# Kernel optimization log

Measured on AMD Instinct MI355X. Metric: run time of the kernel, lower is better.

The kernel has to match this reference:

```python
import jax, jax.numpy as jnp
import numpy as np

N, M = 50000, 32
HID, FILT, NBR = 128, 128, 64


def setup_inputs() -> dict:
    key = jax.random.key(0)
    ks = jax.random.split(key, 12)
    s = lambda fan_in: 1.0 / np.sqrt(fan_in)
    return {
        "node_repr": jax.random.normal(ks[0], (N, HID), dtype=jnp.float32),
        "nbr_fea": jax.random.normal(ks[1], (N, M, NBR), dtype=jnp.float32),
        "nbr_fea_idx": jax.random.randint(ks[2], (N, M), 0, N, dtype=jnp.int64),
        # filter_net: Linear(NBR, FILT) -> SiLU -> Linear(FILT, HID)
        "fw1": jax.random.uniform(ks[3], (NBR, FILT), jnp.float32, -s(NBR), s(NBR)),
        "fb1": jax.random.uniform(ks[4], (FILT,), jnp.float32, -s(NBR), s(NBR)),
        "fw2": jax.random.uniform(ks[5], (FILT, HID), jnp.float32, -s(FILT), s(FILT)),
        "fb2": jax.random.uniform(ks[6], (HID,), jnp.float32, -s(FILT), s(FILT)),
        # update: Linear(HID, HID) -> SiLU -> Linear(HID, HID)
        "uw1": jax.random.uniform(ks[7], (HID, HID), jnp.float32, -s(HID), s(HID)),
        "ub1": jax.random.uniform(ks[8], (HID,), jnp.float32, -s(HID), s(HID)),
        "uw2": jax.random.uniform(ks[9], (HID, HID), jnp.float32, -s(HID), s(HID)),
        "ub2": jax.random.uniform(ks[10], (HID,), jnp.float32, -s(HID), s(HID)),
    }


def reference(node_repr, nbr_fea, nbr_fea_idx, fw1, fb1, fw2, fb2, uw1, ub1, uw2, ub2):
    # gather neighbor representations: [N, M, HID]
    neighbor_repr = node_repr[nbr_fea_idx]
    # continuous filters from neighbor features: [N, M, HID]
    h = jax.nn.silu(jnp.einsum("nmf,fk->nmk", nbr_fea, fw1) + fb1)
    filters = jnp.einsum("nmk,kh->nmh", h, fw2) + fb2
    # filter-weighted sum over neighbors: [N, HID]
    message = jnp.sum(neighbor_repr * filters, axis=1)
    # update MLP
    u = jax.nn.silu(message @ uw1 + ub1)
    return u @ uw2 + ub2
```

## Files before the change

kernel.cpp:

```cpp
#include <hip/hip_runtime.h>


#define NN 50000
#define MM 32
#define HID 128
#define NBR 64

typedef __attribute__((ext_vector_type(4))) float f32x4;
typedef __attribute__((ext_vector_type(8))) short s16x8;
typedef __attribute__((ext_vector_type(4))) short s16x4;

__device__ __forceinline__ short f2bf(float x) {
  unsigned u = __builtin_bit_cast(unsigned, x);
  unsigned r = (u + 0x7FFFu + ((u >> 16) & 1u)) >> 16;
  return (short)r;
}

__device__ __forceinline__ float silu(float x) {
  return x / (1.0f + __expf(-x));
}

__global__ __launch_bounds__(512, 2) void k_filter_message(
    const float* __restrict__ node_repr, const float* __restrict__ nbr_fea,
    const int* __restrict__ nbr_idx, const float* __restrict__ fw1,
    const float* __restrict__ fb1, const float* __restrict__ fw2,
    const float* __restrict__ fb2, float* __restrict__ msg_out)
{
  __shared__ __align__(16) short s_w1[128 * 72];
  __shared__ __align__(16) short s_w2[128 * 136];
  __shared__ float s_b1[128];
  __shared__ float s_b2[128];
  __shared__ __align__(16) float s_filt[8 * 16 * 132];

  const int tid = threadIdx.x;
  for (int i = tid; i < 64 * 128; i += 512) {
    int k = i >> 7, f = i & 127;
    s_w1[f * 72 + k] = f2bf(fw1[i]);
  }
  for (int i = tid; i < 128 * 128; i += 512) {
    int k = i >> 7, h = i & 127;
    s_w2[h * 136 + k] = f2bf(fw2[i]);
  }
  if (tid < 128) { s_b1[tid] = fb1[tid]; s_b2[tid] = fb2[tid]; }
  __syncthreads();

  const int wave = tid >> 6, lane = tid & 63;
  const int c = lane & 15, g = lane >> 4;
  float* __restrict__ ft = s_filt + wave * (16 * 132);
  const int gw = blockIdx.x * 8 + wave;
  const int stride = gridDim.x * 8;

  for (int n = gw; n < NN; n += stride) {
    const float* nf = nbr_fea + (size_t)n * (MM * NBR);

    s16x8 b1[2][2];
    #pragma unroll
    for (int mt = 0; mt < 2; ++mt)
      #pragma unroll
      for (int kt = 0; kt < 2; ++kt) {
        const f32x4* src = reinterpret_cast<const f32x4*>(
            nf + (mt * 16 + c) * NBR + kt * 32 + g * 8);
        f32x4 lo = __builtin_nontemporal_load(src);
        f32x4 hi = __builtin_nontemporal_load(src + 1);
        s16x8 v;
        v[0] = f2bf(lo[0]); v[1] = f2bf(lo[1]); v[2] = f2bf(lo[2]); v[3] = f2bf(lo[3]);
        v[4] = f2bf(hi[0]); v[5] = f2bf(hi[1]); v[6] = f2bf(hi[2]); v[7] = f2bf(hi[3]);
        b1[mt][kt] = v;
      }

    f32x4 acc1[8][2];
    #pragma unroll
    for (int t = 0; t < 8; ++t)
      #pragma unroll
      for (int mt = 0; mt < 2; ++mt)
        acc1[t][mt] = f32x4{0.f, 0.f, 0.f, 0.f};
    #pragma unroll
    for (int kt = 0; kt < 2; ++kt)
      #pragma unroll
      for (int t = 0; t < 8; ++t) {
        s16x8 a1 = *reinterpret_cast<const s16x8*>(&s_w1[(t * 16 + c) * 72 + kt * 32 + g * 8]);
        #pragma unroll
        for (int mt = 0; mt < 2; ++mt)
          acc1[t][mt] = __builtin_amdgcn_mfma_f32_16x16x32_bf16(a1, b1[mt][kt], acc1[t][mt], 0, 0, 0);
      }

    s16x4 P[8][2];
    #pragma unroll
    for (int t = 0; t < 8; ++t)
      #pragma unroll
      for (int mt = 0; mt < 2; ++mt) {
        s16x4 p;
        #pragma unroll
        for (int r = 0; r < 4; ++r) {
          float x = acc1[t][mt][r] + s_b1[t * 16 + g * 4 + r];
          p[r] = f2bf(silu(x));
        }
        P[t][mt] = p;
      }

    f32x4 acc2[8][2];
    #pragma unroll
    for (int ct = 0; ct < 8; ++ct)
      #pragma unroll
      for (int mt = 0; mt < 2; ++mt)
        acc2[ct][mt] = f32x4{0.f, 0.f, 0.f, 0.f};
    #pragma unroll
    for (int ct = 0; ct < 8; ++ct)
      #pragma unroll
      for (int kt = 0; kt < 8; ++kt) {
        s16x4 b2 = *reinterpret_cast<const s16x4*>(&s_w2[(ct * 16 + c) * 136 + kt * 16 + g * 4]);
        #pragma unroll
        for (int mt = 0; mt < 2; ++mt)
          acc2[ct][mt] = __builtin_amdgcn_mfma_f32_16x16x16bf16_1k(P[kt][mt], b2, acc2[ct][mt], 0, 0, 0);
      }

    float msg0 = 0.f, msg1 = 0.f;
    #pragma unroll
    for (int mt = 0; mt < 2; ++mt) {
      #pragma unroll
      for (int ct = 0; ct < 8; ++ct) {
        const float bias = s_b2[ct * 16 + c];
        #pragma unroll
        for (int r = 0; r < 4; ++r)
          ft[(4 * g + r) * 132 + ct * 16 + c] = acc2[ct][mt][r] + bias;
      }
      #pragma unroll
      for (int m = 0; m < 16; ++m) {
        const int idx = nbr_idx[(size_t)n * MM + mt * 16 + m];
        const float2 nr = *reinterpret_cast<const float2*>(
            node_repr + (size_t)idx * HID + 2 * lane);
        const float2 fv = *reinterpret_cast<const float2*>(&ft[m * 132 + 2 * lane]);
        msg0 += fv.x * nr.x;
        msg1 += fv.y * nr.y;
      }
    }
    *reinterpret_cast<float2*>(msg_out + (size_t)n * HID + 2 * lane) =
        float2{msg0, msg1};
  }
}

__global__ __launch_bounds__(256, 2) void k_update1(
    const float* __restrict__ msg, const float* __restrict__ uw1,
    const float* __restrict__ ub1, short* __restrict__ u_out)
{
  __shared__ __align__(16) short s_w1[128 * 136];
  __shared__ float s_b1[128];
  const int tid = threadIdx.x;
  for (int i = tid; i < 128 * 128; i += 256) {
    int k = i >> 7, f = i & 127;
    s_w1[f * 136 + k] = f2bf(uw1[i]);
  }
  if (tid < 128) s_b1[tid] = ub1[tid];
  __syncthreads();

  const int wave = tid >> 6, lane = tid & 63;
  const int c = lane & 15, g = lane >> 4;
  const long base = (long)(blockIdx.x * 4 + wave) * 32;
  if (base >= NN) return;

  s16x8 bfr[2][4];
  #pragma unroll
  for (int mt = 0; mt < 2; ++mt)
    #pragma unroll
    for (int kt = 0; kt < 4; ++kt) {
      long row = base + mt * 16 + c; if (row > NN - 1) row = NN - 1;
      const float* src = msg + row * HID + kt * 32 + g * 8;
      float4 lo = *reinterpret_cast<const float4*>(src);
      float4 hi = *reinterpret_cast<const float4*>(src + 4);
      s16x8 v;
      v[0] = f2bf(lo.x); v[1] = f2bf(lo.y); v[2] = f2bf(lo.z); v[3] = f2bf(lo.w);
      v[4] = f2bf(hi.x); v[5] = f2bf(hi.y); v[6] = f2bf(hi.z); v[7] = f2bf(hi.w);
      bfr[mt][kt] = v;
    }

  f32x4 acc[8][2];
  #pragma unroll
  for (int t = 0; t < 8; ++t)
    #pragma unroll
    for (int mt = 0; mt < 2; ++mt)
      acc[t][mt] = f32x4{0.f, 0.f, 0.f, 0.f};
  #pragma unroll
  for (int kt = 0; kt < 4; ++kt)
    #pragma unroll
    for (int t = 0; t < 8; ++t) {
      s16x8 a = *reinterpret_cast<const s16x8*>(&s_w1[(t * 16 + c) * 136 + kt * 32 + g * 8]);
      #pragma unroll
      for (int mt = 0; mt < 2; ++mt)
        acc[t][mt] = __builtin_amdgcn_mfma_f32_16x16x32_bf16(a, bfr[mt][kt], acc[t][mt], 0, 0, 0);
    }

  #pragma unroll
  for (int t = 0; t < 8; ++t)
    #pragma unroll
    for (int mt = 0; mt < 2; ++mt) {
      long row = base + mt * 16 + c;
      if (row < NN) {
        s16x4 p;
        #pragma unroll
        for (int r = 0; r < 4; ++r) {
          float x = acc[t][mt][r] + s_b1[t * 16 + g * 4 + r];
          p[r] = f2bf(silu(x));
        }
        *reinterpret_cast<s16x4*>(&u_out[row * HID + t * 16 + g * 4]) = p;
      }
    }
}

__global__ __launch_bounds__(256, 2) void k_update2(
    const short* __restrict__ u, const float* __restrict__ uw2,
    const float* __restrict__ ub2, float* __restrict__ out)
{
  __shared__ __align__(16) short s_w2[128 * 136];
  __shared__ float s_b2[128];
  const int tid = threadIdx.x;
  for (int i = tid; i < 128 * 128; i += 256) {
    int k = i >> 7, h = i & 127;
    s_w2[h * 136 + k] = f2bf(uw2[i]);
  }
  if (tid < 128) s_b2[tid] = ub2[tid];
  __syncthreads();

  const int wave = tid >> 6, lane = tid & 63;
  const int c = lane & 15, g = lane >> 4;
  const long base = (long)(blockIdx.x * 4 + wave) * 32;
  if (base >= NN) return;

  s16x4 afr[2][8];
  #pragma unroll
  for (int mt = 0; mt < 2; ++mt)
    #pragma unroll
    for (int kt = 0; kt < 8; ++kt) {
      long row = base + mt * 16 + c; if (row > NN - 1) row = NN - 1;
      afr[mt][kt] = *reinterpret_cast<const s16x4*>(&u[row * HID + kt * 16 + g * 4]);
    }

  f32x4 acc[8][2];
  #pragma unroll
  for (int ct = 0; ct < 8; ++ct)
    #pragma unroll
    for (int mt = 0; mt < 2; ++mt)
      acc[ct][mt] = f32x4{0.f, 0.f, 0.f, 0.f};
  #pragma unroll
  for (int ct = 0; ct < 8; ++ct)
    #pragma unroll
    for (int kt = 0; kt < 8; ++kt) {
      s16x4 b2 = *reinterpret_cast<const s16x4*>(&s_w2[(ct * 16 + c) * 136 + kt * 16 + g * 4]);
      #pragma unroll
      for (int mt = 0; mt < 2; ++mt)
        acc[ct][mt] = __builtin_amdgcn_mfma_f32_16x16x16bf16_1k(afr[mt][kt], b2, acc[ct][mt], 0, 0, 0);
    }

  #pragma unroll
  for (int ct = 0; ct < 8; ++ct) {
    const float bias = s_b2[ct * 16 + c];
    #pragma unroll
    for (int mt = 0; mt < 2; ++mt)
      #pragma unroll
      for (int r = 0; r < 4; ++r) {
        long row = base + mt * 16 + g * 4 + r;
        if (row < NN) out[row * HID + ct * 16 + c] = acc[ct][mt][r] + bias;
      }
  }
}

extern "C" void kernel_launch(void* const* d_in, const int* in_sizes, int n_in,
                              void* d_out, int out_size, void* d_ws, size_t ws_size,
                              hipStream_t stream) {
  const float* node_repr = (const float*)d_in[0];
  const float* nbr_fea   = (const float*)d_in[1];
  const int*   nbr_idx   = (const int*)d_in[2];
  const float* fw1 = (const float*)d_in[3];
  const float* fb1 = (const float*)d_in[4];
  const float* fw2 = (const float*)d_in[5];
  const float* fb2 = (const float*)d_in[6];
  const float* uw1 = (const float*)d_in[7];
  const float* ub1 = (const float*)d_in[8];
  const float* uw2 = (const float*)d_in[9];
  const float* ub2 = (const float*)d_in[10];
  float* outp = (float*)d_out;
  short* u_ws = (short*)d_ws;

  k_filter_message<<<256, 512, 0, stream>>>(node_repr, nbr_fea, nbr_idx,
                                            fw1, fb1, fw2, fb2, outp);
  const int rowblocks = (NN + 31) / 32;
  const int grid2 = (rowblocks + 3) / 4;
  k_update1<<<grid2, 256, 0, stream>>>(outp, uw1, ub1, u_ws);
  k_update2<<<grid2, 256, 0, stream>>>(u_ws, uw2, ub2, outp);
}
```

Measured before the change: 543.9 us.

## Fuse filter-weighted neighbor reduction into MFMA accumulators, drop LDS staging

The second GEMM is transposed so each lane holds filter values for one neighbor row. The lane multiplies them by its gathered node_repr values in registers, then reduces across the 16 neighbors with DPP row sums, so the shared-memory filter staging buffer is no longer needed. Neighbor indices are loaded once per node before the GEMMs. Per-node register pressure drops (one accumulator tile at a time), and the freed LDS allows the grid to grow to 512 blocks. In exchange, node_repr is gathered with a scattered per-lane access pattern, and each output row is written only by the c==0 lanes.

```diff
diff --git a/kernel.cpp b/kernel.cpp
--- a/kernel.cpp
+++ b/kernel.cpp
@@ -18,6 +18,23 @@
 
 __device__ __forceinline__ float silu(float x) {
   return x / (1.0f + __expf(-x));
+}
+
+__device__ __forceinline__ float rowsum16(float x) {
+  int v = __builtin_bit_cast(int, x);
+  v = __builtin_bit_cast(int,
+      __builtin_bit_cast(float, v) +
+      __builtin_bit_cast(float, __builtin_amdgcn_update_dpp(0, v, 0xB1, 0xF, 0xF, false)));
+  v = __builtin_bit_cast(int,
+      __builtin_bit_cast(float, v) +
+      __builtin_bit_cast(float, __builtin_amdgcn_update_dpp(0, v, 0x4E, 0xF, 0xF, false)));
+  v = __builtin_bit_cast(int,
+      __builtin_bit_cast(float, v) +
+      __builtin_bit_cast(float, __builtin_amdgcn_update_dpp(0, v, 0x124, 0xF, 0xF, false)));
+  v = __builtin_bit_cast(int,
+      __builtin_bit_cast(float, v) +
+      __builtin_bit_cast(float, __builtin_amdgcn_update_dpp(0, v, 0x128, 0xF, 0xF, false)));
+  return __builtin_bit_cast(float, v);
 }
 
 __global__ __launch_bounds__(512, 2) void k_filter_message(
@@ -29,8 +46,7 @@
   __shared__ __align__(16) short s_w1[128 * 72];
   __shared__ __align__(16) short s_w2[128 * 136];
   __shared__ float s_b1[128];
-  __shared__ float s_b2[128];
-  __shared__ __align__(16) float s_filt[8 * 16 * 132];
+  __shared__ __align__(16) float s_b2[128];
 
   const int tid = threadIdx.x;
   for (int i = tid; i < 64 * 128; i += 512) {
@@ -46,12 +62,14 @@
 
   const int wave = tid >> 6, lane = tid & 63;
   const int c = lane & 15, g = lane >> 4;
-  float* __restrict__ ft = s_filt + wave * (16 * 132);
   const int gw = blockIdx.x * 8 + wave;
   const int stride = gridDim.x * 8;
 
   for (int n = gw; n < NN; n += stride) {
     const float* nf = nbr_fea + (size_t)n * (MM * NBR);
+
+    int idx0 = nbr_idx[(size_t)n * MM + c];
+    int idx1 = nbr_idx[(size_t)n * MM + 16 + c];
 
     s16x8 b1[2][2];
     #pragma unroll
@@ -68,74 +86,59 @@
         b1[mt][kt] = v;
       }
 
-    f32x4 acc1[8][2];
-    #pragma unroll
-    for (int t = 0; t < 8; ++t)
-      #pragma unroll
-      for (int mt = 0; mt < 2; ++mt)
-        acc1[t][mt] = f32x4{0.f, 0.f, 0.f, 0.f};
-    #pragma unroll
-    for (int kt = 0; kt < 2; ++kt)
-      #pragma unroll
-      for (int t = 0; t < 8; ++t) {
-        s16x8 a1 = *reinterpret_cast<const s16x8*>(&s_w1[(t * 16 + c) * 72 + kt * 32 + g * 8]);
+    s16x4 P[8][2];
+    #pragma unroll
+    for (int t = 0; t < 8; ++t) {
+      f32x4 a0 = f32x4{0.f, 0.f, 0.f, 0.f};
+      f32x4 a1 = f32x4{0.f, 0.f, 0.f, 0.f};
+      #pragma unroll
+      for (int kt = 0; kt < 2; ++kt) {
+        s16x8 w1f = *reinterpret_cast<const s16x8*>(&s_w1[(t * 16 + c) * 72 + kt * 32 + g * 8]);
+        a0 = __builtin_amdgcn_mfma_f32_16x16x32_bf16(w1f, b1[0][kt], a0, 0, 0, 0);
+        a1 = __builtin_amdgcn_mfma_f32_16x16x32_bf16(w1f, b1[1][kt], a1, 0, 0, 0);
+      }
+      s16x4 p0, p1;
+      #pragma unroll
+      for (int r = 0; r < 4; ++r) {
+        float bias = s_b1[t * 16 + g * 4 + r];
+        p0[r] = f2bf(silu(a0[r] + bias));
+        p1[r] = f2bf(silu(a1[r] + bias));
+      }
+      P[t][0] = p0;
+      P[t][1] = p1;
+    }
+
+    f32x4 pacc[8];
+    #pragma unroll
+    for (int ct = 0; ct < 8; ++ct) pacc[ct] = f32x4{0.f, 0.f, 0.f, 0.f};
+
+    #pragma unroll
+    for (int mt = 0; mt < 2; ++mt) {
+      const float* nrp = node_repr + (size_t)(mt ? idx1 : idx0) * HID;
+      #pragma unroll
+      for (int ct = 0; ct < 8; ++ct) {
+        f32x4 acc2t = f32x4{0.f, 0.f, 0.f, 0.f};
         #pragma unroll
-        for (int mt = 0; mt < 2; ++mt)
-          acc1[t][mt] = __builtin_amdgcn_mfma_f32_16x16x32_bf16(a1, b1[mt][kt], acc1[t][mt], 0, 0, 0);
-      }
-
-    s16x4 P[8][2];
-    #pragma unroll
-    for (int t = 0; t < 8; ++t)
-      #pragma unroll
-      for (int mt = 0; mt < 2; ++mt) {
-        s16x4 p;
-        #pragma unroll
-        for (int r = 0; r < 4; ++r) {
-          float x = acc1[t][mt][r] + s_b1[t * 16 + g * 4 + r];
-          p[r] = f2bf(silu(x));
+        for (int kt = 0; kt < 8; ++kt) {
+          s16x4 w2f = *reinterpret_cast<const s16x4*>(&s_w2[(ct * 16 + c) * 136 + kt * 16 + g * 4]);
+          acc2t = __builtin_amdgcn_mfma_f32_16x16x16bf16_1k(w2f, P[kt][mt], acc2t, 0, 0, 0);
         }
-        P[t][mt] = p;
-      }
-
-    f32x4 acc2[8][2];
-    #pragma unroll
-    for (int ct = 0; ct < 8; ++ct)
-      #pragma unroll
-      for (int mt = 0; mt < 2; ++mt)
-        acc2[ct][mt] = f32x4{0.f, 0.f, 0.f, 0.f};
-    #pragma unroll
-    for (int ct = 0; ct < 8; ++ct)
-      #pragma unroll
-      for (int kt = 0; kt < 8; ++kt) {
-        s16x4 b2 = *reinterpret_cast<const s16x4*>(&s_w2[(ct * 16 + c) * 136 + kt * 16 + g * 4]);
-        #pragma unroll
-        for (int mt = 0; mt < 2; ++mt)
-          acc2[ct][mt] = __builtin_amdgcn_mfma_f32_16x16x16bf16_1k(P[kt][mt], b2, acc2[ct][mt], 0, 0, 0);
-      }
-
-    float msg0 = 0.f, msg1 = 0.f;
-    #pragma unroll
-    for (int mt = 0; mt < 2; ++mt) {
-      #pragma unroll
-      for (int ct = 0; ct < 8; ++ct) {
-        const float bias = s_b2[ct * 16 + c];
+        f32x4 nr = *reinterpret_cast<const f32x4*>(nrp + ct * 16 + 4 * g);
+        f32x4 fb = *reinterpret_cast<const f32x4*>(&s_b2[ct * 16 + 4 * g]);
         #pragma unroll
         for (int r = 0; r < 4; ++r)
-          ft[(4 * g + r) * 132 + ct * 16 + c] = acc2[ct][mt][r] + bias;
-      }
-      #pragma unroll
-      for (int m = 0; m < 16; ++m) {
-        const int idx = nbr_idx[(size_t)n * MM + mt * 16 + m];
-        const float2 nr = *reinterpret_cast<const float2*>(
-            node_repr + (size_t)idx * HID + 2 * lane);
-        const float2 fv = *reinterpret_cast<const float2*>(&ft[m * 132 + 2 * lane]);
-        msg0 += fv.x * nr.x;
-        msg1 += fv.y * nr.y;
-      }
-    }
-    *reinterpret_cast<float2*>(msg_out + (size_t)n * HID + 2 * lane) =
-        float2{msg0, msg1};
+          pacc[ct][r] += (acc2t[r] + fb[r]) * nr[r];
+      }
+    }
+
+    #pragma unroll
+    for (int ct = 0; ct < 8; ++ct) {
+      f32x4 s;
+      #pragma unroll
+      for (int r = 0; r < 4; ++r) s[r] = rowsum16(pacc[ct][r]);
+      if (c == 0)
+        *reinterpret_cast<f32x4*>(msg_out + (size_t)n * HID + ct * 16 + 4 * g) = s;
+    }
   }
 }
 
@@ -280,7 +283,7 @@
   float* outp = (float*)d_out;
   short* u_ws = (short*)d_ws;
 
-  k_filter_message<<<256, 512, 0, stream>>>(node_repr, nbr_fea, nbr_idx,
+  k_filter_message<<<512, 512, 0, stream>>>(node_repr, nbr_fea, nbr_idx,
                                             fw1, fb1, fw2, fb2, outp);
   const int rowblocks = (NN + 31) / 32;
   const int grid2 = (rowblocks + 3) / 4;
```

New measurement: 525.7 us. 1.03x faster.
